# Kernel tuning notes

Measured on AMD Instinct MI355X. Metric: run time of the kernel, lower is better.

The kernel has to match this reference:

```python
import jax, jax.numpy as jnp
import numpy as np

B, S, H = 1, 2048, 2048
NH, NKV, HD = 16, 4, 128
N_REP = NH // NKV
WINDOW = 1024
THETA = 10000.0


def _rope(x, fc):
    # x: [B,S,h,HD]; fc: [B,S,HD//2,2] (cos,sin)
    xr = x.reshape(*x.shape[:-1], HD // 2, 2)
    a, b = xr[..., 0], xr[..., 1]
    cos = fc[:, :, None, :, 0]
    sin = fc[:, :, None, :, 1]
    out = jnp.stack((a * cos - b * sin, a * sin + b * cos), axis=-1)
    return out.reshape(x.shape)


def setup_inputs() -> dict:
    key = jax.random.key(0)
    ks = jax.random.split(key, 5)
    hidden_state = jax.random.normal(ks[0], (B, S, H), jnp.float32)
    # rotary table: cos/sin of pos * theta^{-2i/d}
    inv_freq = 1.0 / (THETA ** (jnp.arange(0, HD, 2, dtype=jnp.float32) / HD))
    ang = jnp.arange(S, dtype=jnp.float32)[:, None] * inv_freq[None, :]  # [S, HD//2]
    freq_cis = jnp.stack((jnp.cos(ang), jnp.sin(ang)), axis=-1)  # [S, HD//2, 2]
    attention_mask = jnp.ones((B, S), dtype=bool)
    i = jnp.arange(S)[:, None]
    j = jnp.arange(S)[None, :]
    causal_mask = ((j <= i) & (i - j < WINDOW))[None, None]  # [1,1,S,S] sliding-window causal
    position_ids = jnp.broadcast_to(jnp.arange(S, dtype=jnp.int32), (B, S))
    scale = 0.02
    Wq = jax.random.normal(ks[1], (H, NH * HD), jnp.float32) * scale
    Wk = jax.random.normal(ks[2], (H, NKV * HD), jnp.float32) * scale
    Wv = jax.random.normal(ks[3], (H, NKV * HD), jnp.float32) * scale
    Wo = jax.random.normal(ks[4], (NH * HD, H), jnp.float32) * scale
    return {"hidden_state": hidden_state, "freq_cis": freq_cis,
            "attention_mask": attention_mask, "causal_mask": causal_mask,
            "position_ids": position_ids, "Wq": Wq, "Wk": Wk, "Wv": Wv, "Wo": Wo}


def reference(hidden_state, freq_cis, attention_mask, causal_mask, position_ids,
              Wq, Wk, Wv, Wo):
    q = (hidden_state @ Wq).reshape(B, S, NH, HD)
    k = (hidden_state @ Wk).reshape(B, S, NKV, HD)
    v = (hidden_state @ Wv).reshape(B, S, NKV, HD)
    fc = freq_cis[position_ids]  # [B,S,HD//2,2]
    q = _rope(q, fc)
    k = _rope(k, fc)
    # GQA: repeat kv heads (contiguous groups, as in repeat_kv)
    k = jnp.repeat(k, N_REP, axis=2)  # [B,S,NH,HD]
    v = jnp.repeat(v, N_REP, axis=2)
    mask = causal_mask & attention_mask[:, None, None, :]  # [B,1,S,S]
    bias = jnp.where(mask, 0.0, jnp.finfo(jnp.float32).min)
    scores = jnp.einsum('bqhd,bkhd->bhqk', q, k) * (1.0 / np.sqrt(HD))
    attn = jax.nn.softmax(scores + bias, axis=-1)
    out = jnp.einsum('bhqk,bkhd->bqhd', attn, v).reshape(B, S, NH * HD)
    return out @ Wo
```

## Files before the change

kernel.cpp:

```cpp
#include <hip/hip_runtime.h>
#include <hip/hip_bf16.h>
#include <stdint.h>

#define S_LEN 2048
#define HDIM  2048
#define NHQ   16
#define NKVH  4
#define HD    128
#define WIN   1024
#define QKV_N 3072
#define SM_SCALE 0.08838834764831845f
#define NEG_BIG  -1.0e30f

typedef __attribute__((ext_vector_type(8))) short short8;
typedef __attribute__((ext_vector_type(4))) float float4v;
typedef unsigned short u16;

static __device__ __forceinline__ float bf2f(u16 u) {
  union { unsigned int i; float f; } v; v.i = ((unsigned int)u) << 16; return v.f;
}
static __device__ __forceinline__ u16 f2bf(float f) {
  union { float f; unsigned int i; } v; v.f = f;
  unsigned int x = v.i;
  return (u16)((x + 0x7fffu + ((x >> 16) & 1u)) >> 16);
}

__global__ __launch_bounds__(256) void hs_pack(
    const float* __restrict__ x, u16* __restrict__ y)
{
  const int b = blockIdx.x;
  u16* dst = y + (size_t)b * 4096;
  const int mb = b >> 6, ks = b & 63;
#pragma unroll
  for (int i = 0; i < 2; ++i) {
    const int cid = i * 256 + threadIdx.x;
    const int kc  = cid & 3;
    const int m   = cid >> 2;
    const float* src = x + ((size_t)(mb * 128 + m)) * 2048 + ks * 32 + kc * 8;
    const float4 v0 = *(const float4*)src;
    const float4 v1 = *(const float4*)(src + 4);
    short8 o;
    o[0] = (short)f2bf(v0.x); o[1] = (short)f2bf(v0.y);
    o[2] = (short)f2bf(v0.z); o[3] = (short)f2bf(v0.w);
    o[4] = (short)f2bf(v1.x); o[5] = (short)f2bf(v1.y);
    o[6] = (short)f2bf(v1.z); o[7] = (short)f2bf(v1.w);
    *(short8*)(dst + (kc * 128 + m) * 8) = o;
  }
}

__global__ __launch_bounds__(256) void wtrans_all(
    const float* __restrict__ Wq, const float* __restrict__ Wk,
    const float* __restrict__ Wv, const float* __restrict__ Wo,
    u16* __restrict__ WqkvT, u16* __restrict__ WoT)
{
  __shared__ u16 t[32][33];
  const int tx = threadIdx.x & 31, ty = threadIdx.x >> 5;
  const int k0 = blockIdx.y * 32;
  const int n0 = blockIdx.x * 32;

  const float* W; u16* DT; int nsrc, N;
  if (blockIdx.z == 0) {
    if (n0 < 2048)      { W = Wq; nsrc = n0;        N = 2048; }
    else if (n0 < 2560) { W = Wk; nsrc = n0 - 2048; N = 512;  }
    else                { W = Wv; nsrc = n0 - 2560; N = 512;  }
    DT = WqkvT;
  } else {
    if (n0 >= 2048) return;
    W = Wo; nsrc = n0; N = 2048; DT = WoT;
  }

#pragma unroll
  for (int i = 0; i < 4; ++i)
    t[ty + i * 8][tx] = f2bf(W[(size_t)(k0 + ty + i * 8) * N + nsrc + tx]);
  __syncthreads();
  const int kstep = blockIdx.y;
  const int kc = tx >> 3, e = tx & 7;
#pragma unroll
  for (int i = 0; i < 4; ++i) {
    const int n = n0 + ty + i * 8;
    DT[((size_t)((n >> 6) * 64 + kstep)) * 2048 + kc * 512 + (n & 63) * 8 + e]
        = t[tx][ty + i * 8];
  }
}

template <bool OUT_F32>
__global__ __launch_bounds__(256) void gemm_bt(
    const u16* __restrict__ Apk, const u16* __restrict__ Bpk,
    void* __restrict__ Cv, int M, int N, int K)
{
  __shared__ u16 Als[4096];
  __shared__ u16 Bls[2048];

  const int tid  = threadIdx.x;
  const int lane = tid & 63;
  const int w    = tid >> 6;
  const int quad = lane >> 4;
  const int lc   = lane & 15;
  const int n0   = blockIdx.x * 64;
  const int m0   = blockIdx.y * 128;
  const int wr   = (w >> 1) * 64;
  const int wc   = (w & 1) * 32;
  const int ktiles = K >> 5;

  float4v acc[4][2];
#pragma unroll
  for (int i = 0; i < 4; ++i)
#pragma unroll
    for (int j = 0; j < 2; ++j) acc[i][j] = (float4v){0.f, 0.f, 0.f, 0.f};

  for (int ks = 0; ks < ktiles; ++ks) {
    const char* ab = (const char*)(Apk + ((size_t)((m0 >> 7) * ktiles + ks)) * 4096);
    const char* bb = (const char*)(Bpk + ((size_t)((n0 >> 6) * ktiles + ks)) * 2048);
    __syncthreads();
#pragma unroll
    for (int r = 0; r < 2; ++r) {
      const int off = r * 4096 + tid * 16;
      __builtin_amdgcn_global_load_lds(
          (__attribute__((address_space(1))) void*)(ab + off),
          (__attribute__((address_space(3))) void*)((char*)Als + off), 16, 0, 0);
    }
    {
      const int off = tid * 16;
      __builtin_amdgcn_global_load_lds(
          (__attribute__((address_space(1))) void*)(bb + off),
          (__attribute__((address_space(3))) void*)((char*)Bls + off), 16, 0, 0);
    }
    __syncthreads();

    short8 af[4], bfr[2];
#pragma unroll
    for (int mi = 0; mi < 4; ++mi)
      af[mi] = *(const short8*)(Als + quad * 1024 + (wr + mi * 16 + lc) * 8);
#pragma unroll
    for (int ni = 0; ni < 2; ++ni)
      bfr[ni] = *(const short8*)(Bls + quad * 512 + (wc + ni * 16 + lc) * 8);
#pragma unroll
    for (int mi = 0; mi < 4; ++mi)
#pragma unroll
      for (int ni = 0; ni < 2; ++ni)
        acc[mi][ni] = __builtin_amdgcn_mfma_f32_16x16x32_bf16(
            af[mi], bfr[ni], acc[mi][ni], 0, 0, 0);
  }

#pragma unroll
  for (int mi = 0; mi < 4; ++mi)
#pragma unroll
    for (int ni = 0; ni < 2; ++ni)
#pragma unroll
      for (int r = 0; r < 4; ++r) {
        const int row = m0 + wr + mi * 16 + quad * 4 + r;
        const int col = n0 + wc + ni * 16 + lc;
        if (OUT_F32)
          ((float*)Cv)[(size_t)row * N + col] = acc[mi][ni][r];
        else
          ((u16*)Cv)[(size_t)row * N + col] = f2bf(acc[mi][ni][r]);
      }
}

__global__ __launch_bounds__(256) void rope_pack(
    u16* __restrict__ qkv, const float* __restrict__ fc,
    u16* __restrict__ kp)
{
  const int b = blockIdx.x;
  if (b < 1024) {
    const int t    = b * 256 + threadIdx.x;
    const int row  = t >> 7;
    const int head = (t & 127) >> 3;
    const int d0   = (t & 7) * 8;
    u16* p = qkv + (size_t)row * QKV_N + head * HD + 2 * d0;
    short8 v0 = *(const short8*)p;
    short8 v1 = *(const short8*)(p + 8);
    const float2* f = (const float2*)(fc + row * 128) + d0;
    short8 o0, o1;
#pragma unroll
    for (int u = 0; u < 4; ++u) {
      const float2 cs = f[u];
      const float a = bf2f((u16)v0[2 * u]), bb = bf2f((u16)v0[2 * u + 1]);
      o0[2 * u]     = (short)f2bf(a * cs.x - bb * cs.y);
      o0[2 * u + 1] = (short)f2bf(a * cs.y + bb * cs.x);
    }
#pragma unroll
    for (int u = 0; u < 4; ++u) {
      const float2 cs = f[4 + u];
      const float a = bf2f((u16)v1[2 * u]), bb = bf2f((u16)v1[2 * u + 1]);
      o1[2 * u]     = (short)f2bf(a * cs.x - bb * cs.y);
      o1[2 * u + 1] = (short)f2bf(a * cs.y + bb * cs.x);
    }
    *(short8*)p = o0;
    *(short8*)(p + 8) = o1;
  } else {
    const int bb2 = b - 1024;
    const int kvh = bb2 >> 5;
    const int kt  = bb2 & 31;
    u16* dst = kp + ((size_t)(kvh * 32 + kt)) * 64 * 128;
#pragma unroll
    for (int i = 0; i < 4; ++i) {
      const int cid = i * 256 + threadIdx.x;
      const int key = cid >> 4;
      const int c   = cid & 15;
      const int s   = kt * 64 + key;
      short8 v = *(const short8*)(qkv + (size_t)s * QKV_N + 2048 + kvh * HD + c * 8);
      const float2* f = (const float2*)(fc + s * 128) + c * 4;
      short8 o;
#pragma unroll
      for (int u = 0; u < 4; ++u) {
        const float2 cs = f[u];
        const float a = bf2f((u16)v[2 * u]), bb3 = bf2f((u16)v[2 * u + 1]);
        o[2 * u]     = (short)f2bf(a * cs.x - bb3 * cs.y);
        o[2 * u + 1] = (short)f2bf(a * cs.y + bb3 * cs.x);
      }
      *(short8*)(dst + key * 128 + ((c ^ (key & 15)) * 8)) = o;
    }
  }
}

__global__ __launch_bounds__(256) void vpack_kernel(
    const u16* __restrict__ qkv, u16* __restrict__ vp)
{
  __shared__ u16 t[32][33];
  const int s0  = blockIdx.x * 32;
  const int h0  = blockIdx.y * 32;
  const int kvh = blockIdx.z;
  const int tx = threadIdx.x & 31, ty = threadIdx.x >> 5;
  const int kt   = s0 >> 6;
  const int keyb = s0 & 63;
#pragma unroll
  for (int i = 0; i < 4; ++i)
    t[ty + i * 8][tx] = qkv[(size_t)(s0 + ty + i * 8) * QKV_N + 2560 + kvh * HD + h0 + tx];
  __syncthreads();
  u16* dst = vp + ((size_t)(kvh * 32 + kt)) * 128 * 64;
#pragma unroll
  for (int i = 0; i < 4; ++i) {
    const int hd   = h0 + ty + i * 8;
    const int keyl = keyb + tx;
    const int c    = (keyl >> 3) ^ (hd & 7);
    dst[hd * 64 + c * 8 + (keyl & 7)] = t[tx][ty + i * 8];
  }
}

__global__ __launch_bounds__(256) void attn_kernel(
    const u16* __restrict__ qkv, const u16* __restrict__ kp,
    const u16* __restrict__ vp, u16* __restrict__ out)
{
  __shared__ u16 Kls[64 * 128];
  __shared__ u16 Vls[128 * 64];
  __shared__ u16 P[4 * 16 * 72];

  const int tid  = threadIdx.x;
  const int lane = tid & 63;
  const int w    = tid >> 6;
  const int quad = lane >> 4;
  const int lc   = lane & 15;
  const int q0   = blockIdx.x * 64;
  const int h    = blockIdx.y;
  const int kvh  = h >> 2;
  const int rb   = q0 + w * 16;

  short8 qf[4];
  {
    const u16* qp = qkv + (size_t)(rb + lc) * QKV_N + h * HD + quad * 8;
#pragma unroll
    for (int ks = 0; ks < 4; ++ks) qf[ks] = *(const short8*)(qp + ks * 32);
  }

  float4v o[8];
#pragma unroll
  for (int i = 0; i < 8; ++i) o[i] = (float4v){0.f, 0.f, 0.f, 0.f};
  float mrow[4], lrow[4];
#pragma unroll
  for (int r = 0; r < 4; ++r) { mrow[r] = NEG_BIG; lrow[r] = 0.f; }

  int jmin_blk = q0 - (WIN - 1); if (jmin_blk < 0) jmin_blk = 0;
  const int kt_begin = jmin_blk >> 6;
  const int kt_end   = q0 >> 6;

  const size_t tbase = (size_t)(kvh * 32) * 64 * 128;

  for (int kt = kt_begin; kt <= kt_end; ++kt) {
    const int k0 = kt * 64;

    __syncthreads();
    {
      const u16* kg = kp + tbase + (size_t)kt * 64 * 128;
      const u16* vg = vp + tbase + (size_t)kt * 128 * 64;
#pragma unroll
      for (int i = 0; i < 4; ++i) {
        const int off = i * 4096 + tid * 16;
        __builtin_amdgcn_global_load_lds(
            (__attribute__((address_space(1))) void*)((const char*)kg + off),
            (__attribute__((address_space(3))) void*)((char*)Kls + off), 16, 0, 0);
        __builtin_amdgcn_global_load_lds(
            (__attribute__((address_space(1))) void*)((const char*)vg + off),
            (__attribute__((address_space(3))) void*)((char*)Vls + off), 16, 0, 0);
      }
    }
    __syncthreads();

    if (k0 > rb + 15 || k0 + 63 < rb - (WIN - 1)) continue;

    float4v sacc[4];
#pragma unroll
    for (int i = 0; i < 4; ++i) sacc[i] = (float4v){0.f, 0.f, 0.f, 0.f};
#pragma unroll
    for (int ks = 0; ks < 4; ++ks) {
#pragma unroll
      for (int nt = 0; nt < 4; ++nt) {
        const int key = nt * 16 + lc;
        const int c   = (ks * 4 + quad) ^ (key & 15);
        short8 kb = *(const short8*)(Kls + key * 128 + c * 8);
        sacc[nt] = __builtin_amdgcn_mfma_f32_16x16x32_bf16(qf[ks], kb, sacc[nt], 0, 0, 0);
      }
    }

    const bool full = (k0 + 63 <= rb) && ((rb + 15 - k0) <= WIN - 1);
    float sv[4][4];
    bool  ok[4][4];
    float rmax[4] = {NEG_BIG, NEG_BIG, NEG_BIG, NEG_BIG};
#pragma unroll
    for (int nt = 0; nt < 4; ++nt) {
      const int j = k0 + nt * 16 + lc;
#pragma unroll
      for (int r = 0; r < 4; ++r) {
        const int i = rb + quad * 4 + r;
        const bool valid = full || ((j <= i) && (i - j < WIN));
        float s = sacc[nt][r] * SM_SCALE;
        s = valid ? s : NEG_BIG;
        sv[nt][r] = s;
        ok[nt][r] = valid;
        rmax[r] = fmaxf(rmax[r], s);
      }
    }
#pragma unroll
    for (int off = 1; off < 16; off <<= 1)
#pragma unroll
      for (int r = 0; r < 4; ++r)
        rmax[r] = fmaxf(rmax[r], __shfl_xor(rmax[r], off, 64));

    float alpha[4], rsum[4];
#pragma unroll
    for (int r = 0; r < 4; ++r) {
      const float mn = fmaxf(mrow[r], rmax[r]);
      alpha[r] = __expf(mrow[r] - mn);
      mrow[r] = mn;
      rsum[r] = 0.f;
    }
#pragma unroll
    for (int nt = 0; nt < 4; ++nt)
#pragma unroll
      for (int r = 0; r < 4; ++r) {
        const float p = ok[nt][r] ? __expf(sv[nt][r] - mrow[r]) : 0.f;
        rsum[r] += p;
        P[(w * 16 + quad * 4 + r) * 72 + nt * 16 + lc] = f2bf(p);
      }
#pragma unroll
    for (int off = 1; off < 16; off <<= 1)
#pragma unroll
      for (int r = 0; r < 4; ++r)
        rsum[r] += __shfl_xor(rsum[r], off, 64);
#pragma unroll
    for (int r = 0; r < 4; ++r) lrow[r] = lrow[r] * alpha[r] + rsum[r];
#pragma unroll
    for (int i = 0; i < 8; ++i)
#pragma unroll
      for (int r = 0; r < 4; ++r) o[i][r] *= alpha[r];

#pragma unroll
    for (int ktk = 0; ktk < 2; ++ktk) {
      short8 pa = *(const short8*)(P + (w * 16 + lc) * 72 + ktk * 32 + quad * 8);
#pragma unroll
      for (int nt2 = 0; nt2 < 8; ++nt2) {
        const int hd = nt2 * 16 + lc;
        const int c  = (ktk * 4 + quad) ^ (hd & 7);
        short8 vb = *(const short8*)(Vls + hd * 64 + c * 8);
        o[nt2] = __builtin_amdgcn_mfma_f32_16x16x32_bf16(pa, vb, o[nt2], 0, 0, 0);
      }
    }
  }

#pragma unroll
  for (int r = 0; r < 4; ++r) {
    const float inv = (lrow[r] > 0.f) ? (1.f / lrow[r]) : 0.f;
    const int row = rb + quad * 4 + r;
    const size_t mbase = (size_t)(row >> 7) * 64;
    const int m = row & 127;
#pragma unroll
    for (int nt2 = 0; nt2 < 8; ++nt2) {
      const int col = h * HD + nt2 * 16 + lc;
      const int kstep = col >> 5, kc = (col >> 3) & 3, e = col & 7;
      out[(mbase + kstep) * 4096 + kc * 1024 + m * 8 + e] = f2bf(o[nt2][r] * inv);
    }
  }
}

extern "C" void kernel_launch(void* const* d_in, const int* in_sizes, int n_in,
                              void* d_out, int out_size, void* d_ws, size_t ws_size,
                              hipStream_t stream) {
  const float* hs = (const float*)d_in[0];
  const float* fc = (const float*)d_in[1];
  const float* Wq = (const float*)d_in[5];
  const float* Wk = (const float*)d_in[6];
  const float* Wv = (const float*)d_in[7];
  const float* Wo = (const float*)d_in[8];
  float* outp = (float*)d_out;

  u16* hsB   = (u16*)d_ws;
  u16* WqkvT = hsB   + (size_t)2048 * 2048;
  u16* WoT   = WqkvT + (size_t)3072 * 2048;
  u16* QKV   = WoT   + (size_t)2048 * 2048;
  u16* ATTN  = QKV   + (size_t)2048 * 3072;
  u16* Kp    = ATTN  + (size_t)2048 * 2048;
  u16* Vp    = Kp    + (size_t)4 * 2048 * 128;

  dim3 blk(256);
  hs_pack<<<dim3(1024), blk, 0, stream>>>(hs, hsB);
  wtrans_all<<<dim3(96, 64, 2), blk, 0, stream>>>(Wq, Wk, Wv, Wo, WqkvT, WoT);

  gemm_bt<false><<<dim3(3072 / 64, 2048 / 128), blk, 0, stream>>>(hsB, WqkvT, QKV, 2048, 3072, 2048);
  rope_pack<<<dim3(1152), blk, 0, stream>>>(QKV, fc, Kp);
  vpack_kernel<<<dim3(64, 4, NKVH), blk, 0, stream>>>(QKV, Vp);
  attn_kernel<<<dim3(2048 / 64, NHQ), blk, 0, stream>>>(QKV, Kp, Vp, ATTN);
  gemm_bt<true><<<dim3(2048 / 64, 2048 / 128), blk, 0, stream>>>(ATTN, WoT, outp, 2048, 2048, 2048);
}
```

Measured before the change: 265.7 us.

## Fuse RoPE and K/V packing into QKV GEMM epilogue; merge prep kernels

The hidden-state bf16 pack and weight transpose kernels are merged into a single prep launch. RoPE on Q and K, the swizzled K layout, and the transposed V packing move into the QKV GEMM epilogue, which uses a lane shuffle to pair rotary elements. This drops the full QKV intermediate round trip and two launches. In exchange the epilogue does scattered 2-byte stores and per-element freq loads, which may be less coalesced than the old dedicated pack kernels.

Result: no change. 262.7 us (-1.1%).

```diff
diff --git a/kernel.cpp b/kernel.cpp
--- a/kernel.cpp
+++ b/kernel.cpp
@@ -8,7 +8,6 @@
 #define NKVH  4
 #define HD    128
 #define WIN   1024
-#define QKV_N 3072
 #define SM_SCALE 0.08838834764831845f
 #define NEG_BIG  -1.0e30f
 
@@ -25,55 +24,58 @@
   return (u16)((x + 0x7fffu + ((x >> 16) & 1u)) >> 16);
 }
 
-__global__ __launch_bounds__(256) void hs_pack(
-    const float* __restrict__ x, u16* __restrict__ y)
+__global__ __launch_bounds__(256) void prep(
+    const float* __restrict__ hs, const float* __restrict__ Wq,
+    const float* __restrict__ Wk, const float* __restrict__ Wv,
+    const float* __restrict__ Wo, u16* __restrict__ hsB,
+    u16* __restrict__ WqkvT, u16* __restrict__ WoT)
 {
   const int b = blockIdx.x;
-  u16* dst = y + (size_t)b * 4096;
-  const int mb = b >> 6, ks = b & 63;
-#pragma unroll
-  for (int i = 0; i < 2; ++i) {
-    const int cid = i * 256 + threadIdx.x;
-    const int kc  = cid & 3;
-    const int m   = cid >> 2;
-    const float* src = x + ((size_t)(mb * 128 + m)) * 2048 + ks * 32 + kc * 8;
-    const float4 v0 = *(const float4*)src;
-    const float4 v1 = *(const float4*)(src + 4);
-    short8 o;
-    o[0] = (short)f2bf(v0.x); o[1] = (short)f2bf(v0.y);
-    o[2] = (short)f2bf(v0.z); o[3] = (short)f2bf(v0.w);
-    o[4] = (short)f2bf(v1.x); o[5] = (short)f2bf(v1.y);
-    o[6] = (short)f2bf(v1.z); o[7] = (short)f2bf(v1.w);
-    *(short8*)(dst + (kc * 128 + m) * 8) = o;
-  }
-}
-
-__global__ __launch_bounds__(256) void wtrans_all(
-    const float* __restrict__ Wq, const float* __restrict__ Wk,
-    const float* __restrict__ Wv, const float* __restrict__ Wo,
-    u16* __restrict__ WqkvT, u16* __restrict__ WoT)
-{
+  if (b < 1024) {
+    u16* dst = hsB + (size_t)b * 4096;
+    const int mb = b >> 6, ks = b & 63;
+#pragma unroll
+    for (int i = 0; i < 2; ++i) {
+      const int cid = i * 256 + threadIdx.x;
+      const int kc  = cid & 3;
+      const int m   = cid >> 2;
+      const float* src = hs + ((size_t)(mb * 128 + m)) * 2048 + ks * 32 + kc * 8;
+      const float4 v0 = *(const float4*)src;
+      const float4 v1 = *(const float4*)(src + 4);
+      short8 o;
+      o[0] = (short)f2bf(v0.x); o[1] = (short)f2bf(v0.y);
+      o[2] = (short)f2bf(v0.z); o[3] = (short)f2bf(v0.w);
+      o[4] = (short)f2bf(v1.x); o[5] = (short)f2bf(v1.y);
+      o[6] = (short)f2bf(v1.z); o[7] = (short)f2bf(v1.w);
+      *(short8*)(dst + (kc * 128 + m) * 8) = o;
+    }
+    return;
+  }
+
   __shared__ u16 t[32][33];
   const int tx = threadIdx.x & 31, ty = threadIdx.x >> 5;
-  const int k0 = blockIdx.y * 32;
-  const int n0 = blockIdx.x * 32;
-
+  int n0, kstep;
   const float* W; u16* DT; int nsrc, N;
-  if (blockIdx.z == 0) {
+  if (b < 7168) {
+    const int bb = b - 1024;
+    n0    = (bb % 96) * 32;
+    kstep = bb / 96;
     if (n0 < 2048)      { W = Wq; nsrc = n0;        N = 2048; }
     else if (n0 < 2560) { W = Wk; nsrc = n0 - 2048; N = 512;  }
     else                { W = Wv; nsrc = n0 - 2560; N = 512;  }
     DT = WqkvT;
   } else {
-    if (n0 >= 2048) return;
+    const int bb = b - 7168;
+    n0    = (bb & 63) * 32;
+    kstep = bb >> 6;
     W = Wo; nsrc = n0; N = 2048; DT = WoT;
   }
+  const int k0 = kstep * 32;
 
 #pragma unroll
   for (int i = 0; i < 4; ++i)
     t[ty + i * 8][tx] = f2bf(W[(size_t)(k0 + ty + i * 8) * N + nsrc + tx]);
   __syncthreads();
-  const int kstep = blockIdx.y;
   const int kc = tx >> 3, e = tx & 7;
 #pragma unroll
   for (int i = 0; i < 4; ++i) {
@@ -83,10 +85,12 @@
   }
 }
 
-template <bool OUT_F32>
+template <int EPI>
 __global__ __launch_bounds__(256) void gemm_bt(
     const u16* __restrict__ Apk, const u16* __restrict__ Bpk,
-    void* __restrict__ Cv, int M, int N, int K)
+    void* __restrict__ Cv, const float* __restrict__ fc,
+    u16* __restrict__ Qb, u16* __restrict__ Kp, u16* __restrict__ Vp,
+    int M, int N, int K)
 {
   __shared__ u16 Als[4096];
   __shared__ u16 Bls[2048];
@@ -142,104 +146,65 @@
             af[mi], bfr[ni], acc[mi][ni], 0, 0, 0);
   }
 
-#pragma unroll
-  for (int mi = 0; mi < 4; ++mi)
-#pragma unroll
-    for (int ni = 0; ni < 2; ++ni)
-#pragma unroll
-      for (int r = 0; r < 4; ++r) {
-        const int row = m0 + wr + mi * 16 + quad * 4 + r;
-        const int col = n0 + wc + ni * 16 + lc;
-        if (OUT_F32)
+  if (EPI == 0) {
+#pragma unroll
+    for (int mi = 0; mi < 4; ++mi)
+#pragma unroll
+      for (int ni = 0; ni < 2; ++ni)
+#pragma unroll
+        for (int r = 0; r < 4; ++r) {
+          const int row = m0 + wr + mi * 16 + quad * 4 + r;
+          const int col = n0 + wc + ni * 16 + lc;
           ((float*)Cv)[(size_t)row * N + col] = acc[mi][ni][r];
-        else
-          ((u16*)Cv)[(size_t)row * N + col] = f2bf(acc[mi][ni][r]);
-      }
-}
-
-__global__ __launch_bounds__(256) void rope_pack(
-    u16* __restrict__ qkv, const float* __restrict__ fc,
-    u16* __restrict__ kp)
-{
-  const int b = blockIdx.x;
-  if (b < 1024) {
-    const int t    = b * 256 + threadIdx.x;
-    const int row  = t >> 7;
-    const int head = (t & 127) >> 3;
-    const int d0   = (t & 7) * 8;
-    u16* p = qkv + (size_t)row * QKV_N + head * HD + 2 * d0;
-    short8 v0 = *(const short8*)p;
-    short8 v1 = *(const short8*)(p + 8);
-    const float2* f = (const float2*)(fc + row * 128) + d0;
-    short8 o0, o1;
-#pragma unroll
-    for (int u = 0; u < 4; ++u) {
-      const float2 cs = f[u];
-      const float a = bf2f((u16)v0[2 * u]), bb = bf2f((u16)v0[2 * u + 1]);
-      o0[2 * u]     = (short)f2bf(a * cs.x - bb * cs.y);
-      o0[2 * u + 1] = (short)f2bf(a * cs.y + bb * cs.x);
-    }
-#pragma unroll
-    for (int u = 0; u < 4; ++u) {
-      const float2 cs = f[4 + u];
-      const float a = bf2f((u16)v1[2 * u]), bb = bf2f((u16)v1[2 * u + 1]);
-      o1[2 * u]     = (short)f2bf(a * cs.x - bb * cs.y);
-      o1[2 * u + 1] = (short)f2bf(a * cs.y + bb * cs.x);
-    }
-    *(short8*)p = o0;
-    *(short8*)(p + 8) = o1;
+        }
   } else {
-    const int bb2 = b - 1024;
-    const int kvh = bb2 >> 5;
-    const int kt  = bb2 & 31;
-    u16* dst = kp + ((size_t)(kvh * 32 + kt)) * 64 * 128;
-#pragma unroll
-    for (int i = 0; i < 4; ++i) {
-      const int cid = i * 256 + threadIdx.x;
-      const int key = cid >> 4;
-      const int c   = cid & 15;
-      const int s   = kt * 64 + key;
-      short8 v = *(const short8*)(qkv + (size_t)s * QKV_N + 2048 + kvh * HD + c * 8);
-      const float2* f = (const float2*)(fc + s * 128) + c * 4;
-      short8 o;
-#pragma unroll
-      for (int u = 0; u < 4; ++u) {
-        const float2 cs = f[u];
-        const float a = bf2f((u16)v[2 * u]), bb3 = bf2f((u16)v[2 * u + 1]);
-        o[2 * u]     = (short)f2bf(a * cs.x - bb3 * cs.y);
-        o[2 * u + 1] = (short)f2bf(a * cs.y + bb3 * cs.x);
-      }
-      *(short8*)(dst + key * 128 + ((c ^ (key & 15)) * 8)) = o;
-    }
-  }
-}
-
-__global__ __launch_bounds__(256) void vpack_kernel(
-    const u16* __restrict__ qkv, u16* __restrict__ vp)
-{
-  __shared__ u16 t[32][33];
-  const int s0  = blockIdx.x * 32;
-  const int h0  = blockIdx.y * 32;
-  const int kvh = blockIdx.z;
-  const int tx = threadIdx.x & 31, ty = threadIdx.x >> 5;
-  const int kt   = s0 >> 6;
-  const int keyb = s0 & 63;
-#pragma unroll
-  for (int i = 0; i < 4; ++i)
-    t[ty + i * 8][tx] = qkv[(size_t)(s0 + ty + i * 8) * QKV_N + 2560 + kvh * HD + h0 + tx];
-  __syncthreads();
-  u16* dst = vp + ((size_t)(kvh * 32 + kt)) * 128 * 64;
-#pragma unroll
-  for (int i = 0; i < 4; ++i) {
-    const int hd   = h0 + ty + i * 8;
-    const int keyl = keyb + tx;
-    const int c    = (keyl >> 3) ^ (hd & 7);
-    dst[hd * 64 + c * 8 + (keyl & 7)] = t[tx][ty + i * 8];
+    if (n0 < 2560) {
+#pragma unroll
+      for (int mi = 0; mi < 4; ++mi)
+#pragma unroll
+        for (int ni = 0; ni < 2; ++ni)
+#pragma unroll
+          for (int r = 0; r < 4; ++r) {
+            const int row = m0 + wr + mi * 16 + quad * 4 + r;
+            const int col = n0 + wc + ni * 16 + lc;
+            const int hh  = col & 127;
+            const float v = acc[mi][ni][r];
+            const float p = __shfl_xor(v, 1);
+            const float2 cs = *(const float2*)(fc + row * 128 + (hh & ~1));
+            const float res = (col & 1) ? (p * cs.y + v * cs.x)
+                                        : (v * cs.x - p * cs.y);
+            if (n0 < 2048) {
+              Qb[(size_t)row * 2048 + col] = f2bf(res);
+            } else {
+              const int kvh = (col - 2048) >> 7;
+              const int kt  = row >> 6, key = row & 63;
+              const int c   = hh >> 3, e = hh & 7;
+              Kp[((size_t)(kvh * 32 + kt)) * 8192 + key * 128
+                 + ((c ^ (key & 15)) * 8) + e] = f2bf(res);
+            }
+          }
+    } else {
+#pragma unroll
+      for (int mi = 0; mi < 4; ++mi)
+#pragma unroll
+        for (int ni = 0; ni < 2; ++ni)
+#pragma unroll
+          for (int r = 0; r < 4; ++r) {
+            const int row = m0 + wr + mi * 16 + quad * 4 + r;
+            const int col = n0 + wc + ni * 16 + lc;
+            const int kvh = (col - 2560) >> 7;
+            const int hd  = col & 127;
+            const int kt  = row >> 6, key = row & 63;
+            const int c   = (key >> 3) ^ (hd & 7);
+            Vp[((size_t)(kvh * 32 + kt)) * 8192 + hd * 64 + c * 8 + (key & 7)]
+                = f2bf(acc[mi][ni][r]);
+          }
+    }
   }
 }
 
 __global__ __launch_bounds__(256) void attn_kernel(
-    const u16* __restrict__ qkv, const u16* __restrict__ kp,
+    const u16* __restrict__ Qb, const u16* __restrict__ kp,
     const u16* __restrict__ vp, u16* __restrict__ out)
 {
   __shared__ u16 Kls[64 * 128];
@@ -258,7 +223,7 @@
 
   short8 qf[4];
   {
-    const u16* qp = qkv + (size_t)(rb + lc) * QKV_N + h * HD + quad * 8;
+    const u16* qp = Qb + (size_t)(rb + lc) * 2048 + h * HD + quad * 8;
 #pragma unroll
     for (int ks = 0; ks < 4; ++ks) qf[ks] = *(const short8*)(qp + ks * 32);
   }
@@ -274,15 +239,15 @@
   const int kt_begin = jmin_blk >> 6;
   const int kt_end   = q0 >> 6;
 
-  const size_t tbase = (size_t)(kvh * 32) * 64 * 128;
+  const size_t tbase = (size_t)(kvh * 32) * 8192;
 
   for (int kt = kt_begin; kt <= kt_end; ++kt) {
     const int k0 = kt * 64;
 
     __syncthreads();
     {
-      const u16* kg = kp + tbase + (size_t)kt * 64 * 128;
-      const u16* vg = vp + tbase + (size_t)kt * 128 * 64;
+      const u16* kg = kp + tbase + (size_t)kt * 8192;
+      const u16* vg = vp + tbase + (size_t)kt * 8192;
 #pragma unroll
       for (int i = 0; i < 4; ++i) {
         const int off = i * 4096 + tid * 16;
@@ -406,18 +371,16 @@
   u16* hsB   = (u16*)d_ws;
   u16* WqkvT = hsB   + (size_t)2048 * 2048;
   u16* WoT   = WqkvT + (size_t)3072 * 2048;
-  u16* QKV   = WoT   + (size_t)2048 * 2048;
-  u16* ATTN  = QKV   + (size_t)2048 * 3072;
+  u16* Qb    = WoT   + (size_t)2048 * 2048;
+  u16* ATTN  = Qb    + (size_t)2048 * 2048;
   u16* Kp    = ATTN  + (size_t)2048 * 2048;
   u16* Vp    = Kp    + (size_t)4 * 2048 * 128;
 
   dim3 blk(256);
-  hs_pack<<<dim3(1024), blk, 0, stream>>>(hs, hsB);
-  wtrans_all<<<dim3(96, 64, 2), blk, 0, stream>>>(Wq, Wk, Wv, Wo, WqkvT, WoT);
-
-  gemm_bt<false><<<dim3(3072 / 64, 2048 / 128), blk, 0, stream>>>(hsB, WqkvT, QKV, 2048, 3072, 2048);
-  rope_pack<<<dim3(1152), blk, 0, stream>>>(QKV, fc, Kp);
-  vpack_kernel<<<dim3(64, 4, NKVH), blk, 0, stream>>>(QKV, Vp);
-  attn_kernel<<<dim3(2048 / 64, NHQ), blk, 0, stream>>>(QKV, Kp, Vp, ATTN);
-  gemm_bt<true><<<dim3(2048 / 64, 2048 / 128), blk, 0, stream>>>(ATTN, WoT, outp, 2048, 2048, 2048);
-}
+  prep<<<dim3(11264), blk, 0, stream>>>(hs, Wq, Wk, Wv, Wo, hsB, WqkvT, WoT);
+  gemm_bt<1><<<dim3(3072 / 64, 2048 / 128), blk, 0, stream>>>(
+      hsB, WqkvT, nullptr, fc, Qb, Kp, Vp, 2048, 3072, 2048);
+  attn_kernel<<<dim3(2048 / 64, NHQ), blk, 0, stream>>>(Qb, Kp, Vp, ATTN);
+  gemm_bt<0><<<dim3(2048 / 64, 2048 / 128), blk, 0, stream>>>(
+      ATTN, WoT, outp, nullptr, nullptr, nullptr, nullptr, 2048, 2048, 2048);
+}
```
